# Kernel optimization log

Hardware: AMD Instinct MI355X
Metric: run time of the kernel (lower is better)

## Reference

```python
import jax, jax.numpy as jnp
import numpy as np

RES = 2048
IN = 3
OUT = 2
THRESHOLD = 1.0
BETA = 0.9
SPECTRAL_RADIUS = 0.9


def _make_W(rng):
    # random recurrent matrix scaled to target spectral radius (power iteration estimate)
    W = rng.standard_normal((RES, RES)).astype(np.float32)
    v = rng.standard_normal(RES).astype(np.float32)
    lam = 1.0
    for _ in range(100):
        v = W @ v
        lam = np.linalg.norm(v)
        v = v / (lam + 1e-12)
    return W * (SPECTRAL_RADIUS / lam)


def _xavier(rng, fan_out, fan_in):
    bound = np.sqrt(6.0 / (fan_in + fan_out))
    return rng.uniform(-bound, bound, (fan_out, fan_in)).astype(np.float32)


def setup_inputs() -> dict:
    key = jax.random.key(0)
    rng = np.random.default_rng(42)
    x = jax.random.normal(key, (200, 256, IN), dtype=jnp.float32)
    W = jnp.asarray(_make_W(rng))            # [RES, RES] recurrent weights
    Win = jnp.asarray(_xavier(rng, RES, IN))  # [RES, IN]  input_layer.weight
    Wout = jnp.asarray(_xavier(rng, OUT, RES))  # [OUT, RES] readout.weight
    return {"x": x, "W": W, "Win": Win, "Wout": Wout}


def reference(x, W, Win, Wout):
    seq_len, batch, _ = x.shape
    res = W.shape[0]

    def step(carry, x_t):
        V, S = carry
        # leaky integrate: input current + recurrent current
        V_new = BETA * V + x_t @ Win.T + S @ W  # [batch, res]
        S_new = (V_new >= THRESHOLD).astype(V.dtype)
        V_new = V_new * (1.0 - S_new)  # reset_mechanism == 'zero'
        return (V_new, S_new), S_new

    init = (jnp.zeros((batch, res), x.dtype), jnp.zeros((batch, res), x.dtype))
    _, spk_rec = jax.lax.scan(step, init, x)  # [seq, batch, res]
    spk_avg = spk_rec[-10:].mean(axis=0)       # [batch, res]
    logits = spk_avg @ Wout.T                  # [batch, out]
    return spk_rec, logits
```

## Files before the change

### kernel.cpp

```cpp
#include <hip/hip_runtime.h>


#define SEQ    200
#define BATCH  256
#define NRES   2048
#define NTHR   1024
#define BETA_F 0.9f

__global__ __launch_bounds__(NTHR, 1) void snn_reservoir_kernel(
    const float* __restrict__ x,
    const float* __restrict__ W,
    const float* __restrict__ Win,
    const float* __restrict__ Wout,
    float* __restrict__ out)
{
    const int b    = blockIdx.x;
    const int tid  = threadIdx.x;
    const int lane = tid & 63;
    const int wid  = tid >> 6;
    const int n0   = tid << 1;

    __shared__ unsigned long long smask[2][32];
    __shared__ int   scum[2];
    __shared__ float4 sx[SEQ];
    __shared__ float red[2][16];

    for (int t = tid; t < SEQ; t += NTHR) {
        const float* p = x + (size_t)t * (BATCH * 3) + b * 3;
        sx[t] = make_float4(p[0], p[1], p[2], 0.0f);
    }
    if (tid < 64) smask[tid >> 5][tid & 31] = 0ull;
    if (tid < 2)  scum[tid] = 0;

    const float* wr = Win + (size_t)n0 * 3;
    const float w00 = wr[0], w01 = wr[1], w02 = wr[2];
    const float w10 = wr[3], w11 = wr[4], w12 = wr[5];

    float V0 = 0.f, V1 = 0.f;
    int cnt0 = 0, cnt1 = 0;

    __syncthreads();

    auto step = [&](int t, int cur, int prev, int& seen) {
        float rec0 = 0.f, rec1 = 0.f;
        const int c = scum[prev];
        if (__builtin_expect(c != seen, 0)) {
            seen = c;
            #pragma unroll 1
            for (int u = 0; u < 32; ++u) {
                unsigned long long m = smask[prev][u];
                const int kbase = ((u >> 1) << 7) + (u & 1);
                while (m) {
                    const int l = __builtin_ctzll(m);
                    m &= m - 1;
                    const int k = kbase + (l << 1);
                    const float2 wv = *(const float2*)(W + (size_t)k * NRES + n0);
                    rec0 += wv.x;
                    rec1 += wv.y;
                }
            }
        }
        const float4 xv = sx[t];
        const float i0 = fmaf(xv.x, w00, fmaf(xv.y, w01, xv.z * w02)) + rec0;
        const float i1 = fmaf(xv.x, w10, fmaf(xv.y, w11, xv.z * w12)) + rec1;
        V0 = fmaf(BETA_F, V0, i0);
        V1 = fmaf(BETA_F, V1, i1);
        const bool s0 = (V0 >= 1.0f);
        const bool s1 = (V1 >= 1.0f);
        V0 = s0 ? 0.f : V0;
        V1 = s1 ? 0.f : V1;
        *(float2*)(out + ((size_t)t * BATCH + b) * NRES + n0) =
            make_float2(s0 ? 1.f : 0.f, s1 ? 1.f : 0.f);
        if (t >= SEQ - 10) { cnt0 += (int)s0; cnt1 += (int)s1; }
        const unsigned long long b0 = __ballot(s0);
        const unsigned long long b1 = __ballot(s1);
        if (lane == 0) {
            smask[cur][2 * wid]     = b0;
            smask[cur][2 * wid + 1] = b1;
            const int pc = __popcll(b0) + __popcll(b1);
            if (pc) atomicAdd(&scum[cur], pc);
        }
        asm volatile("s_waitcnt lgkmcnt(0)\n\ts_barrier" ::: "memory");
    };

    int seen0 = 0, seen1 = 0;
    for (int tt = 0; tt < SEQ; tt += 2) {
        step(tt,     0, 1, seen1);
        step(tt + 1, 1, 0, seen0);
    }

    const float a0 = (float)cnt0 * 0.1f;
    const float a1 = (float)cnt1 * 0.1f;
    float p0 = fmaf(a0, Wout[n0], a1 * Wout[n0 + 1]);
    float p1 = fmaf(a0, Wout[NRES + n0], a1 * Wout[NRES + n0 + 1]);
    #pragma unroll
    for (int off = 32; off > 0; off >>= 1) {
        p0 += __shfl_down(p0, off);
        p1 += __shfl_down(p1, off);
    }
    if (lane == 0) { red[0][wid] = p0; red[1][wid] = p1; }
    __syncthreads();
    if (tid == 0) {
        float q0 = 0.f, q1 = 0.f;
        #pragma unroll
        for (int i = 0; i < 16; ++i) { q0 += red[0][i]; q1 += red[1][i]; }
        const size_t loff = (size_t)SEQ * BATCH * NRES;
        out[loff + b * 2 + 0] = q0;
        out[loff + b * 2 + 1] = q1;
    }
}

extern "C" void kernel_launch(void* const* d_in, const int* in_sizes, int n_in,
                              void* d_out, int out_size, void* d_ws, size_t ws_size,
                              hipStream_t stream) {
    const float* x    = (const float*)d_in[0];
    const float* W    = (const float*)d_in[1];
    const float* Win  = (const float*)d_in[2];
    const float* Wout = (const float*)d_in[3];
    float* out = (float*)d_out;
    hipLaunchKernelGGL(snn_reservoir_kernel, dim3(BATCH), dim3(NTHR), 0, stream,
                       x, W, Win, Wout, out);
}
```

Before: 409.2 us.

## Add barrier-free input-only fast path, fall back to recurrent sweep on spikes

Each block first simulates all timesteps assuming no recurrent spikes, which is exact while no neuron fires. It writes spikes with nontemporal 64-bit stores and no per-step barriers, and counts nothing. If any neuron in the batch row fired, the block reruns the full barrier-synchronised recurrent simulation, which overwrites the output. The fast path removes 200 block barriers and ballots whenever a row stays silent; otherwise it adds a second full pass of output writes.

```diff
diff --git a/kernel.cpp b/kernel.cpp
--- a/kernel.cpp
+++ b/kernel.cpp
@@ -21,24 +21,65 @@
     const int n0   = tid << 1;
 
     __shared__ unsigned long long smask[2][32];
-    __shared__ int   scum[2];
+    __shared__ int    scum[2];
     __shared__ float4 sx[SEQ];
-    __shared__ float red[2][16];
+    __shared__ float  red[2][16];
+    __shared__ int    sspike;
 
     for (int t = tid; t < SEQ; t += NTHR) {
         const float* p = x + (size_t)t * (BATCH * 3) + b * 3;
         sx[t] = make_float4(p[0], p[1], p[2], 0.0f);
     }
-    if (tid < 64) smask[tid >> 5][tid & 31] = 0ull;
-    if (tid < 2)  scum[tid] = 0;
+    if (tid == 0) sspike = 0;
 
     const float* wr = Win + (size_t)n0 * 3;
     const float w00 = wr[0], w01 = wr[1], w02 = wr[2];
     const float w10 = wr[3], w11 = wr[4], w12 = wr[5];
 
+    __syncthreads();
+
     float V0 = 0.f, V1 = 0.f;
+    bool  any = false;
+    unsigned long long* pout =
+        (unsigned long long*)(out + (size_t)b * NRES + n0);
+    const size_t step_ull = (size_t)BATCH * NRES / 2;
+
+    #pragma unroll 4
+    for (int t = 0; t < SEQ; ++t) {
+        const float4 xv = sx[t];
+        const float i0 = fmaf(xv.x, w00, fmaf(xv.y, w01, xv.z * w02));
+        const float i1 = fmaf(xv.x, w10, fmaf(xv.y, w11, xv.z * w12));
+        V0 = fmaf(BETA_F, V0, i0);
+        V1 = fmaf(BETA_F, V1, i1);
+        const bool s0 = (V0 >= 1.0f);
+        const bool s1 = (V1 >= 1.0f);
+        any |= (s0 | s1);
+        V0 = s0 ? 0.f : V0;
+        V1 = s1 ? 0.f : V1;
+        const unsigned long long wv =
+            ((unsigned long long)(s1 ? 0x3f800000u : 0u) << 32) |
+            (unsigned long long)(s0 ? 0x3f800000u : 0u);
+        __builtin_nontemporal_store(wv, pout);
+        pout += step_ull;
+    }
+
+    const int wany = __any(any);
+    if (wany && lane == 0) atomicOr(&sspike, 1);
+    __syncthreads();
+
+    const size_t loff = (size_t)SEQ * BATCH * NRES;
+    if (sspike == 0) {
+        if (tid == 0) {
+            out[loff + b * 2 + 0] = 0.f;
+            out[loff + b * 2 + 1] = 0.f;
+        }
+        return;
+    }
+
+    if (tid < 64) smask[tid >> 5][tid & 31] = 0ull;
+    if (tid < 2)  scum[tid] = 0;
+    V0 = 0.f; V1 = 0.f;
     int cnt0 = 0, cnt1 = 0;
-
     __syncthreads();
 
     auto step = [&](int t, int cur, int prev, int& seen) {
@@ -54,9 +95,9 @@
                     const int l = __builtin_ctzll(m);
                     m &= m - 1;
                     const int k = kbase + (l << 1);
-                    const float2 wv = *(const float2*)(W + (size_t)k * NRES + n0);
-                    rec0 += wv.x;
-                    rec1 += wv.y;
+                    const float2 wvv = *(const float2*)(W + (size_t)k * NRES + n0);
+                    rec0 += wvv.x;
+                    rec1 += wvv.y;
                 }
             }
         }
@@ -104,7 +145,6 @@
         float q0 = 0.f, q1 = 0.f;
         #pragma unroll
         for (int i = 0; i < 16; ++i) { q0 += red[0][i]; q1 += red[1][i]; }
-        const size_t loff = (size_t)SEQ * BATCH * NRES;
         out[loff + b * 2 + 0] = q0;
         out[loff + b * 2 + 1] = q1;
     }
```

Measured after the change: 425.6 us. 1.04x slower.
